# Kernel tuning notes

Measured on AMD Instinct MI355X. Metric: run time of the kernel, lower is better.

The kernel has to match this reference:

```python
import jax, jax.numpy as jnp
import numpy as np

VOCAB = 50000
D = 256          # vector_dim == hidden size
SEQ = 128
BATCH = 4096
NUM_CLASSES = 5


def setup_inputs() -> dict:
    key = jax.random.key(0)
    ks = jax.random.split(key, 8)
    x = jax.random.randint(ks[0], (BATCH, SEQ), 0, VOCAB, dtype=jnp.int64)
    scale = 1.0 / np.sqrt(D)
    emb = jax.random.normal(ks[1], (VOCAB, D), dtype=jnp.float32)
    emb = emb.at[0].set(0.0)  # padding_idx=0 row is zero
    W_ih = jax.random.uniform(ks[2], (D, D), jnp.float32, -scale, scale)
    W_hh = jax.random.uniform(ks[3], (D, D), jnp.float32, -scale, scale)
    b_ih = jax.random.uniform(ks[4], (D,), jnp.float32, -scale, scale)
    b_hh = jax.random.uniform(ks[5], (D,), jnp.float32, -scale, scale)
    W_cls = jax.random.uniform(ks[6], (NUM_CLASSES, D), jnp.float32, -scale, scale)
    b_cls = jax.random.uniform(ks[7], (NUM_CLASSES,), jnp.float32, -scale, scale)
    return {"x": x, "emb": emb, "W_ih": W_ih, "W_hh": W_hh,
            "b_ih": b_ih, "b_hh": b_hh, "W_cls": W_cls, "b_cls": b_cls}


def reference(x, emb, W_ih, W_hh, b_ih, b_hh, W_cls, b_cls):
    # Embedding lookup: [B, S, D]
    xe = emb[x]
    # Precompute input projections for all timesteps in one GEMM.
    x_proj = jnp.einsum("bsd,hd->bsh", xe, W_ih) + b_ih + b_hh  # [B, S, D]

    def step(h, xp_t):
        h = jnp.tanh(xp_t + h @ W_hh.T)
        return h, None

    h0 = jnp.zeros((x.shape[0], W_hh.shape[0]), dtype=xe.dtype)
    # scan over time axis: [S, B, D]
    h_last, _ = jax.lax.scan(step, h0, jnp.swapaxes(x_proj, 0, 1))
    # classifier on last step
    return h_last @ W_cls.T + b_cls  # [B, 5]
```

## Files before the change

### kernel.cpp

```cpp
#include <hip/hip_runtime.h>


typedef __attribute__((ext_vector_type(8))) short bf16x8;
typedef __attribute__((ext_vector_type(4))) float f32x4;

#define VOCAB 50000
#define NBLK_EMB 256
#define LDS_STRIDE 264

__device__ __align__(256) unsigned short g_P[VOCAB * 256];

static __device__ __forceinline__ float bf2f(unsigned short u) {
    union { unsigned int i; float f; } v; v.i = ((unsigned int)u) << 16; return v.f;
}
static __device__ __forceinline__ float bfbits2f(unsigned int zext_u16) {
    union { unsigned int i; float f; } v; v.i = zext_u16 << 16; return v.f;
}
static __device__ __forceinline__ unsigned short f2bf_rne(float f) {
    union { float f; unsigned int i; } v; v.f = f;
    unsigned int r = v.i + 0x7FFFu + ((v.i >> 16) & 1u);
    return (unsigned short)(r >> 16);
}
static __device__ __forceinline__ unsigned short f2bf_fast(float f) {
    union { float f; unsigned int i; } v; v.f = f;
    return (unsigned short)((v.i + 0x8000u) >> 16);
}
static __device__ __forceinline__ bf16x8 cvt8(float4 a, float4 b) {
    bf16x8 r;
    r[0] = (short)f2bf_rne(a.x); r[1] = (short)f2bf_rne(a.y);
    r[2] = (short)f2bf_rne(a.z); r[3] = (short)f2bf_rne(a.w);
    r[4] = (short)f2bf_rne(b.x); r[5] = (short)f2bf_rne(b.y);
    r[6] = (short)f2bf_rne(b.z); r[7] = (short)f2bf_rne(b.w);
    return r;
}
static __device__ __forceinline__ bf16x8 load8_bf(const float* __restrict__ p) {
    return cvt8(((const float4*)p)[0], ((const float4*)p)[1]);
}
static __device__ __forceinline__ float fast_tanh(float x) {
    x = __builtin_amdgcn_fmed3f(x, -8.f, 8.f);
    float e = __expf(2.f * x);
    return __builtin_fmaf(-2.f, __builtin_amdgcn_rcpf(e + 1.f), 1.f);
}

__global__ __launch_bounds__(256)
void emb_proj_kernel(const float* __restrict__ emb,
                     const float* __restrict__ W_ih,
                     const float* __restrict__ b_ih,
                     const float* __restrict__ b_hh)
{
    __shared__ __align__(16) unsigned short tin [16 * LDS_STRIDE];
    __shared__ __align__(16) unsigned short tout[16 * LDS_STRIDE];
    const int tid  = threadIdx.x;
    const int lane = tid & 63;
    const int wid  = tid >> 6;
    const int n0   = wid * 64;
    const int row  = tid >> 4, seg = tid & 15;

    bf16x8 wf[4][8];
    float  bias[4];
    #pragma unroll
    for (int nt = 0; nt < 4; ++nt) {
        int n = n0 + nt * 16 + (lane & 15);
        bias[nt] = b_ih[n] + b_hh[n];
        #pragma unroll
        for (int kt = 0; kt < 8; ++kt)
            wf[nt][kt] = load8_bf(W_ih + n * 256 + (lane >> 4) * 8 + kt * 32);
    }

    int tile = blockIdx.x;
    float4 a0, a1, a2, a3;
    {
        const float4* s = (const float4*)(emb + ((size_t)tile * 16 + row) * 256 + seg * 16);
        a0 = s[0]; a1 = s[1]; a2 = s[2]; a3 = s[3];
    }

    for (; tile < 3125; tile += NBLK_EMB) {
        *(bf16x8*)(&tin[row * LDS_STRIDE + seg * 16])     = cvt8(a0, a1);
        *(bf16x8*)(&tin[row * LDS_STRIDE + seg * 16 + 8]) = cvt8(a2, a3);
        int tn = tile + NBLK_EMB;
        if (tn < 3125) {
            const float4* s = (const float4*)(emb + ((size_t)tn * 16 + row) * 256 + seg * 16);
            a0 = s[0]; a1 = s[1]; a2 = s[2]; a3 = s[3];
        }
        __syncthreads();

        f32x4 acc[4];
        #pragma unroll
        for (int nt = 0; nt < 4; ++nt) acc[nt] = (f32x4){0.f, 0.f, 0.f, 0.f};
        #pragma unroll
        for (int kt = 0; kt < 8; ++kt) {
            bf16x8 a = *(bf16x8*)(&tin[(lane & 15) * LDS_STRIDE + (lane >> 4) * 8 + kt * 32]);
            #pragma unroll
            for (int nt = 0; nt < 4; ++nt)
                acc[nt] = __builtin_amdgcn_mfma_f32_16x16x32_bf16(a, wf[nt][kt], acc[nt], 0, 0, 0);
        }
        #pragma unroll
        for (int nt = 0; nt < 4; ++nt) {
            int n = n0 + nt * 16 + (lane & 15);
            #pragma unroll
            for (int r = 0; r < 4; ++r)
                tout[((lane >> 4) * 4 + r) * LDS_STRIDE + n] = f2bf_rne(acc[nt][r] + bias[nt]);
        }
        __syncthreads();
        {
            uint4 o0 = *(uint4*)(&tout[row * LDS_STRIDE + seg * 16]);
            uint4 o1 = *(uint4*)(&tout[row * LDS_STRIDE + seg * 16 + 8]);
            uint4* dst = (uint4*)(g_P + ((size_t)tile * 16 + row) * 256 + seg * 16);
            dst[0] = o0; dst[1] = o1;
        }
    }
}

__global__ __launch_bounds__(512, 2)
void rnn_kernel(const int* __restrict__ x,
                const float* __restrict__ W_hh,
                const float* __restrict__ W_cls,
                const float* __restrict__ b_cls,
                float* __restrict__ out)
{
    __shared__ __align__(16) unsigned short h_lds[2][16 * 256];
    __shared__ __align__(16) int tok_t[128 * 16];
    __shared__ __align__(16) float wcls_lds[5 * 256];
    __shared__ float bcls_lds[5];

    const int tid  = threadIdx.x;
    const int lane = tid & 63;
    const int wid  = tid >> 6;
    const int b0   = blockIdx.x * 16;
    const int n0   = wid * 32;
    const int l15  = lane & 15;
    const int quad = lane >> 4;

    bf16x8 wf[2][8];
    #pragma unroll
    for (int nt = 0; nt < 2; ++nt) {
        int n = n0 + nt * 16 + l15;
        #pragma unroll
        for (int kt = 0; kt < 8; ++kt)
            wf[nt][kt] = load8_bf(W_hh + n * 256 + quad * 8 + kt * 32);
    }

    {
        int row = tid & 15, tq = tid >> 4;
        int4 v = *(const int4*)(x + (size_t)(b0 + row) * 128 + tq * 4);
        tok_t[(tq * 4 + 0) * 16 + row] = v.x;
        tok_t[(tq * 4 + 1) * 16 + row] = v.y;
        tok_t[(tq * 4 + 2) * 16 + row] = v.z;
        tok_t[(tq * 4 + 3) * 16 + row] = v.w;
    }
    if (tid < 320) ((float4*)wcls_lds)[tid] = ((const float4*)W_cls)[tid];
    if (tid < 5)   bcls_lds[tid] = b_cls[tid];
    #pragma unroll
    for (int i = 0; i < 4; ++i) ((unsigned int*)h_lds[0])[tid + i * 512] = 0;

    int aoff[8];
    #pragma unroll
    for (int kt = 0; kt < 8; ++kt)
        aoff[kt] = l15 * 512 + (((quad + 4 * kt) ^ l15) << 4);
    int woff[8];
    #pragma unroll
    for (int nt = 0; nt < 2; ++nt)
        #pragma unroll
        for (int r = 0; r < 4; ++r) {
            int row = quad * 4 + r;
            int g   = (n0 >> 3) + nt * 2 + (l15 >> 3);
            woff[nt * 4 + r] = row * 512 + ((g ^ row) << 4) + (l15 & 7) * 2;
        }

    const unsigned int colByte = (unsigned int)(n0 + l15) * 2;

    unsigned int gA[8], gB[8];
    #pragma unroll
    for (int r = 0; r < 4; ++r) {
        const int* xr = x + (size_t)(b0 + quad * 4 + r) * 128;
        const unsigned short* p0 = g_P + (size_t)xr[0] * 256 + n0 + l15;
        const unsigned short* p1 = g_P + (size_t)xr[1] * 256 + n0 + l15;
        gA[r] = p0[0]; gA[4 + r] = p0[16];
        gB[r] = p1[0]; gB[4 + r] = p1[16];
    }
    __syncthreads();

    char* const h0 = (char*)&h_lds[0][0];

    auto step = [&](const char* hA, char* hW, unsigned int* g, int t) {
        f32x4 acc0 = { bfbits2f(g[0]), bfbits2f(g[1]), bfbits2f(g[2]), bfbits2f(g[3]) };
        f32x4 acc1 = { bfbits2f(g[4]), bfbits2f(g[5]), bfbits2f(g[6]), bfbits2f(g[7]) };
        if (t + 2 < 128) {
            int4 tk = *(const int4*)&tok_t[(t + 2) * 16 + quad * 4];
            const unsigned short* r0 = (const unsigned short*)((const char*)g_P + ((unsigned int)tk.x * 512 + colByte));
            const unsigned short* r1 = (const unsigned short*)((const char*)g_P + ((unsigned int)tk.y * 512 + colByte));
            const unsigned short* r2 = (const unsigned short*)((const char*)g_P + ((unsigned int)tk.z * 512 + colByte));
            const unsigned short* r3 = (const unsigned short*)((const char*)g_P + ((unsigned int)tk.w * 512 + colByte));
            g[0] = r0[0]; g[4] = r0[16];
            g[1] = r1[0]; g[5] = r1[16];
            g[2] = r2[0]; g[6] = r2[16];
            g[3] = r3[0]; g[7] = r3[16];
        }
        #pragma unroll
        for (int kt = 0; kt < 8; ++kt) {
            bf16x8 a = *(const bf16x8*)(hA + aoff[kt]);
            acc0 = __builtin_amdgcn_mfma_f32_16x16x32_bf16(a, wf[0][kt], acc0, 0, 0, 0);
            acc1 = __builtin_amdgcn_mfma_f32_16x16x32_bf16(a, wf[1][kt], acc1, 0, 0, 0);
        }
        #pragma unroll
        for (int r = 0; r < 4; ++r) {
            *(unsigned short*)(hW + woff[r])     = f2bf_fast(fast_tanh(acc0[r]));
            *(unsigned short*)(hW + woff[4 + r]) = f2bf_fast(fast_tanh(acc1[r]));
        }
    };

    #pragma unroll 1
    for (int t2 = 0; t2 < 64; ++t2) {
        step(h0,        h0 + 8192, gA, 2 * t2);
        __syncthreads();
        step(h0 + 8192, h0,        gB, 2 * t2 + 1);
        __syncthreads();
    }

    if (tid < 320) {
        int q = tid & 3, p = tid >> 2;
        int row = p / 5, c = p - row * 5;
        float acc = 0.f;
        #pragma unroll
        for (int kk = 0; kk < 64; ++kk) {
            int k = q * 64 + kk;
            int off = row * 512 + ((((k >> 3) ^ row)) << 4) + (k & 7) * 2;
            acc += bf2f(*(const unsigned short*)(h0 + off)) * wcls_lds[c * 256 + k];
        }
        acc += __shfl_xor(acc, 1);
        acc += __shfl_xor(acc, 2);
        if (q == 0) out[(size_t)(b0 + row) * 5 + c] = acc + bcls_lds[c];
    }
}

extern "C" void kernel_launch(void* const* d_in, const int* in_sizes, int n_in,
                              void* d_out, int out_size, void* d_ws, size_t ws_size,
                              hipStream_t stream)
{
    const int*   x     = (const int*)d_in[0];
    const float* emb   = (const float*)d_in[1];
    const float* W_ih  = (const float*)d_in[2];
    const float* W_hh  = (const float*)d_in[3];
    const float* b_ih  = (const float*)d_in[4];
    const float* b_hh  = (const float*)d_in[5];
    const float* W_cls = (const float*)d_in[6];
    const float* b_cls = (const float*)d_in[7];
    float*       out   = (float*)d_out;
    (void)d_ws; (void)ws_size;

    emb_proj_kernel<<<NBLK_EMB, 256, 0, stream>>>(emb, W_ih, b_ih, b_hh);
    rnn_kernel<<<256, 512, 0, stream>>>(x, W_hh, W_cls, b_cls, out);
}
```

Before: 226.1 us.

## Stage projected-input gathers into LDS via async global_load_lds DMA

Replaces the per-thread scattered 2-byte register gathers of the precomputed input projection with 16-byte global_load_lds transfers into a double-buffered LDS tile. Each step issues the next timestep's row fetch, then waits on vmcnt before the barrier, and reads the current timestep's values from LDS through a skewed layout. This cuts the number of tiny global loads per step, but prefetch depth shrinks from two steps to one, and a full vmcnt wait now sits on the serial recurrence path.

```diff
diff --git a/kernel.cpp b/kernel.cpp
--- a/kernel.cpp
+++ b/kernel.cpp
@@ -12,9 +12,6 @@
 
 static __device__ __forceinline__ float bf2f(unsigned short u) {
     union { unsigned int i; float f; } v; v.i = ((unsigned int)u) << 16; return v.f;
-}
-static __device__ __forceinline__ float bfbits2f(unsigned int zext_u16) {
-    union { unsigned int i; float f; } v; v.i = zext_u16 << 16; return v.f;
 }
 static __device__ __forceinline__ unsigned short f2bf_rne(float f) {
     union { float f; unsigned int i; } v; v.f = f;
@@ -40,6 +37,14 @@
     x = __builtin_amdgcn_fmed3f(x, -8.f, 8.f);
     float e = __expf(2.f * x);
     return __builtin_fmaf(-2.f, __builtin_amdgcn_rcpf(e + 1.f), 1.f);
+}
+static __device__ __forceinline__ void dma16(const void* g, void* l) {
+    __builtin_amdgcn_global_load_lds(
+        (const __attribute__((address_space(1))) unsigned int*)g,
+        (__attribute__((address_space(3))) unsigned int*)l, 16, 0, 0);
+}
+static __device__ __forceinline__ void wait_vm0() {
+    __builtin_amdgcn_s_waitcnt(0x0f70);
 }
 
 __global__ __launch_bounds__(256)
@@ -118,7 +123,8 @@
                 const float* __restrict__ b_cls,
                 float* __restrict__ out)
 {
-    __shared__ __align__(16) unsigned short h_lds[2][16 * 256];
+    __shared__ __align__(16) unsigned short h_lds [2][16 * 256];
+    __shared__ __align__(16) unsigned short xp_lds[2][16 * 256];
     __shared__ __align__(16) int tok_t[128 * 16];
     __shared__ __align__(16) float wcls_lds[5 * 256];
     __shared__ float bcls_lds[5];
@@ -166,35 +172,41 @@
             int g   = (n0 >> 3) + nt * 2 + (l15 >> 3);
             woff[nt * 4 + r] = row * 512 + ((g ^ row) << 4) + (l15 & 7) * 2;
         }
-
-    const unsigned int colByte = (unsigned int)(n0 + l15) * 2;
-
-    unsigned int gA[8], gB[8];
-    #pragma unroll
-    for (int r = 0; r < 4; ++r) {
-        const int* xr = x + (size_t)(b0 + quad * 4 + r) * 128;
-        const unsigned short* p0 = g_P + (size_t)xr[0] * 256 + n0 + l15;
-        const unsigned short* p1 = g_P + (size_t)xr[1] * 256 + n0 + l15;
-        gA[r] = p0[0]; gA[4 + r] = p0[16];
-        gB[r] = p1[0]; gB[4 + r] = p1[16];
-    }
+    int xoff[8];
+    #pragma unroll
+    for (int nt = 0; nt < 2; ++nt)
+        #pragma unroll
+        for (int r = 0; r < 4; ++r) {
+            int row = quad * 4 + r, c = n0 + nt * 16 + l15;
+            xoff[nt * 4 + r] = (row >> 1) * 1024 + (row & 1) * 512
+                             + ((((c >> 3) + (row >> 1)) & 31) << 4) + (c & 7) * 2;
+        }
+
+    const int dmarow = 2 * wid + (lane >> 5);
+    const unsigned int dmaseg = (unsigned int)(((lane & 31) - wid) & 31);
+    char* const xbase = (char*)&xp_lds[0][0];
+    const int   wofs  = wid << 10;
+
     __syncthreads();
+    {
+        int tok = tok_t[0 * 16 + dmarow];
+        dma16(g_P + (size_t)tok * 256 + dmaseg * 8, xbase + wofs);
+    }
+    wait_vm0();
+    __syncthreads();
 
     char* const h0 = (char*)&h_lds[0][0];
 
-    auto step = [&](const char* hA, char* hW, unsigned int* g, int t) {
-        f32x4 acc0 = { bfbits2f(g[0]), bfbits2f(g[1]), bfbits2f(g[2]), bfbits2f(g[3]) };
-        f32x4 acc1 = { bfbits2f(g[4]), bfbits2f(g[5]), bfbits2f(g[6]), bfbits2f(g[7]) };
-        if (t + 2 < 128) {
-            int4 tk = *(const int4*)&tok_t[(t + 2) * 16 + quad * 4];
-            const unsigned short* r0 = (const unsigned short*)((const char*)g_P + ((unsigned int)tk.x * 512 + colByte));
-            const unsigned short* r1 = (const unsigned short*)((const char*)g_P + ((unsigned int)tk.y * 512 + colByte));
-            const unsigned short* r2 = (const unsigned short*)((const char*)g_P + ((unsigned int)tk.z * 512 + colByte));
-            const unsigned short* r3 = (const unsigned short*)((const char*)g_P + ((unsigned int)tk.w * 512 + colByte));
-            g[0] = r0[0]; g[4] = r0[16];
-            g[1] = r1[0]; g[5] = r1[16];
-            g[2] = r2[0]; g[6] = r2[16];
-            g[3] = r3[0]; g[7] = r3[16];
+    auto step = [&](const char* hA, char* hW, const char* xR, char* gw, int t) {
+        if (t + 1 < 128) {
+            int tok = tok_t[(t + 1) * 16 + dmarow];
+            dma16(g_P + (size_t)tok * 256 + dmaseg * 8, gw + wofs);
+        }
+        f32x4 acc0, acc1;
+        #pragma unroll
+        for (int r = 0; r < 4; ++r) {
+            acc0[r] = bf2f(*(const unsigned short*)(xR + xoff[r]));
+            acc1[r] = bf2f(*(const unsigned short*)(xR + xoff[4 + r]));
         }
         #pragma unroll
         for (int kt = 0; kt < 8; ++kt) {
@@ -211,9 +223,11 @@
 
     #pragma unroll 1
     for (int t2 = 0; t2 < 64; ++t2) {
-        step(h0,        h0 + 8192, gA, 2 * t2);
-        __syncthreads();
-        step(h0 + 8192, h0,        gB, 2 * t2 + 1);
+        step(h0,        h0 + 8192, xbase,        xbase + 8192, 2 * t2);
+        wait_vm0();
+        __syncthreads();
+        step(h0 + 8192, h0,        xbase + 8192, xbase,        2 * t2 + 1);
+        wait_vm0();
         __syncthreads();
     }
 
```

Result: slower. 248.5 us (+9.9%).

## Halve batch rows per RNN block and launch one projection block per tile

Applied to the files above, without the earlier changes.

The RNN kernel now processes 8 batch rows per block instead of 16, doubling the grid to 512 blocks and raising the launch-bounds occupancy hint to 4 blocks per CU. The MFMA still computes 16 rows, with the upper half zero and ignored, and only lanes for the real rows gather projections and write h. The embedding-projection kernel drops its persistent, software-prefetched loop and launches one block per 16-row vocabulary tile. The aim is to spread the sequential recurrence across more CUs and waves, at the cost of wasting half of each MFMA and losing the prefetch overlap in the projection kernel.

```diff
diff --git a/kernel.cpp b/kernel.cpp
--- a/kernel.cpp
+++ b/kernel.cpp
@@ -5,16 +5,12 @@
 typedef __attribute__((ext_vector_type(4))) float f32x4;
 
 #define VOCAB 50000
-#define NBLK_EMB 256
 #define LDS_STRIDE 264
 
 __device__ __align__(256) unsigned short g_P[VOCAB * 256];
 
 static __device__ __forceinline__ float bf2f(unsigned short u) {
     union { unsigned int i; float f; } v; v.i = ((unsigned int)u) << 16; return v.f;
-}
-static __device__ __forceinline__ float bfbits2f(unsigned int zext_u16) {
-    union { unsigned int i; float f; } v; v.i = zext_u16 << 16; return v.f;
 }
 static __device__ __forceinline__ unsigned short f2bf_rne(float f) {
     union { float f; unsigned int i; } v; v.f = f;
@@ -55,6 +51,7 @@
     const int wid  = tid >> 6;
     const int n0   = wid * 64;
     const int row  = tid >> 4, seg = tid & 15;
+    const int v0   = blockIdx.x * 16;
 
     bf16x8 wf[4][8];
     float  bias[4];
@@ -67,51 +64,41 @@
             wf[nt][kt] = load8_bf(W_ih + n * 256 + (lane >> 4) * 8 + kt * 32);
     }
 
-    int tile = blockIdx.x;
-    float4 a0, a1, a2, a3;
     {
-        const float4* s = (const float4*)(emb + ((size_t)tile * 16 + row) * 256 + seg * 16);
-        a0 = s[0]; a1 = s[1]; a2 = s[2]; a3 = s[3];
-    }
-
-    for (; tile < 3125; tile += NBLK_EMB) {
-        *(bf16x8*)(&tin[row * LDS_STRIDE + seg * 16])     = cvt8(a0, a1);
-        *(bf16x8*)(&tin[row * LDS_STRIDE + seg * 16 + 8]) = cvt8(a2, a3);
-        int tn = tile + NBLK_EMB;
-        if (tn < 3125) {
-            const float4* s = (const float4*)(emb + ((size_t)tn * 16 + row) * 256 + seg * 16);
-            a0 = s[0]; a1 = s[1]; a2 = s[2]; a3 = s[3];
-        }
-        __syncthreads();
-
-        f32x4 acc[4];
-        #pragma unroll
-        for (int nt = 0; nt < 4; ++nt) acc[nt] = (f32x4){0.f, 0.f, 0.f, 0.f};
-        #pragma unroll
-        for (int kt = 0; kt < 8; ++kt) {
-            bf16x8 a = *(bf16x8*)(&tin[(lane & 15) * LDS_STRIDE + (lane >> 4) * 8 + kt * 32]);
-            #pragma unroll
-            for (int nt = 0; nt < 4; ++nt)
-                acc[nt] = __builtin_amdgcn_mfma_f32_16x16x32_bf16(a, wf[nt][kt], acc[nt], 0, 0, 0);
-        }
-        #pragma unroll
-        for (int nt = 0; nt < 4; ++nt) {
-            int n = n0 + nt * 16 + (lane & 15);
-            #pragma unroll
-            for (int r = 0; r < 4; ++r)
-                tout[((lane >> 4) * 4 + r) * LDS_STRIDE + n] = f2bf_rne(acc[nt][r] + bias[nt]);
-        }
-        __syncthreads();
-        {
-            uint4 o0 = *(uint4*)(&tout[row * LDS_STRIDE + seg * 16]);
-            uint4 o1 = *(uint4*)(&tout[row * LDS_STRIDE + seg * 16 + 8]);
-            uint4* dst = (uint4*)(g_P + ((size_t)tile * 16 + row) * 256 + seg * 16);
-            dst[0] = o0; dst[1] = o1;
-        }
-    }
-}
-
-__global__ __launch_bounds__(512, 2)
+        const float* src = emb + (size_t)(v0 + row) * 256 + seg * 16;
+        bf16x8 lo = load8_bf(src), hi = load8_bf(src + 8);
+        *(bf16x8*)(&tin[row * LDS_STRIDE + seg * 16])     = lo;
+        *(bf16x8*)(&tin[row * LDS_STRIDE + seg * 16 + 8]) = hi;
+    }
+    __syncthreads();
+
+    f32x4 acc[4];
+    #pragma unroll
+    for (int nt = 0; nt < 4; ++nt) acc[nt] = (f32x4){0.f, 0.f, 0.f, 0.f};
+    #pragma unroll
+    for (int kt = 0; kt < 8; ++kt) {
+        bf16x8 a = *(bf16x8*)(&tin[(lane & 15) * LDS_STRIDE + (lane >> 4) * 8 + kt * 32]);
+        #pragma unroll
+        for (int nt = 0; nt < 4; ++nt)
+            acc[nt] = __builtin_amdgcn_mfma_f32_16x16x32_bf16(a, wf[nt][kt], acc[nt], 0, 0, 0);
+    }
+    #pragma unroll
+    for (int nt = 0; nt < 4; ++nt) {
+        int n = n0 + nt * 16 + (lane & 15);
+        #pragma unroll
+        for (int r = 0; r < 4; ++r)
+            tout[((lane >> 4) * 4 + r) * LDS_STRIDE + n] = f2bf_rne(acc[nt][r] + bias[nt]);
+    }
+    __syncthreads();
+    {
+        uint4 o0 = *(uint4*)(&tout[row * LDS_STRIDE + seg * 16]);
+        uint4 o1 = *(uint4*)(&tout[row * LDS_STRIDE + seg * 16 + 8]);
+        uint4* dst = (uint4*)(g_P + (size_t)(v0 + row) * 256 + seg * 16);
+        dst[0] = o0; dst[1] = o1;
+    }
+}
+
+__global__ __launch_bounds__(512, 4)
 void rnn_kernel(const int* __restrict__ x,
                 const float* __restrict__ W_hh,
                 const float* __restrict__ W_cls,
@@ -119,14 +106,14 @@
                 float* __restrict__ out)
 {
     __shared__ __align__(16) unsigned short h_lds[2][16 * 256];
-    __shared__ __align__(16) int tok_t[128 * 16];
+    __shared__ __align__(16) int tok_t[128 * 8];
     __shared__ __align__(16) float wcls_lds[5 * 256];
     __shared__ float bcls_lds[5];
 
     const int tid  = threadIdx.x;
     const int lane = tid & 63;
     const int wid  = tid >> 6;
-    const int b0   = blockIdx.x * 16;
+    const int b0   = blockIdx.x * 8;
     const int n0   = wid * 32;
     const int l15  = lane & 15;
     const int quad = lane >> 4;
@@ -140,18 +127,18 @@
             wf[nt][kt] = load8_bf(W_hh + n * 256 + quad * 8 + kt * 32);
     }
 
-    {
-        int row = tid & 15, tq = tid >> 4;
+    if (tid < 256) {
+        int row = tid & 7, tq = tid >> 3;
         int4 v = *(const int4*)(x + (size_t)(b0 + row) * 128 + tq * 4);
-        tok_t[(tq * 4 + 0) * 16 + row] = v.x;
-        tok_t[(tq * 4 + 1) * 16 + row] = v.y;
-        tok_t[(tq * 4 + 2) * 16 + row] = v.z;
-        tok_t[(tq * 4 + 3) * 16 + row] = v.w;
+        tok_t[(tq * 4 + 0) * 8 + row] = v.x;
+        tok_t[(tq * 4 + 1) * 8 + row] = v.y;
+        tok_t[(tq * 4 + 2) * 8 + row] = v.z;
+        tok_t[(tq * 4 + 3) * 8 + row] = v.w;
     }
     if (tid < 320) ((float4*)wcls_lds)[tid] = ((const float4*)W_cls)[tid];
     if (tid < 5)   bcls_lds[tid] = b_cls[tid];
     #pragma unroll
-    for (int i = 0; i < 4; ++i) ((unsigned int*)h_lds[0])[tid + i * 512] = 0;
+    for (int i = 0; i < 8; ++i) ((unsigned int*)h_lds[0])[tid + i * 512] = 0;
 
     int aoff[8];
     #pragma unroll
@@ -167,26 +154,32 @@
             woff[nt * 4 + r] = row * 512 + ((g ^ row) << 4) + (l15 & 7) * 2;
         }
 
+    unsigned int gA[8] = {0,0,0,0,0,0,0,0};
+    unsigned int gB[8] = {0,0,0,0,0,0,0,0};
+    if (quad < 2) {
+        #pragma unroll
+        for (int r = 0; r < 4; ++r) {
+            const int* xr = x + (size_t)(b0 + quad * 4 + r) * 128;
+            const unsigned short* p0 = g_P + (size_t)xr[0] * 256 + n0 + l15;
+            const unsigned short* p1 = g_P + (size_t)xr[1] * 256 + n0 + l15;
+            gA[r] = p0[0]; gA[4 + r] = p0[16];
+            gB[r] = p1[0]; gB[4 + r] = p1[16];
+        }
+    }
+    __syncthreads();
+
+    char* const h0 = (char*)&h_lds[0][0];
     const unsigned int colByte = (unsigned int)(n0 + l15) * 2;
 
-    unsigned int gA[8], gB[8];
-    #pragma unroll
-    for (int r = 0; r < 4; ++r) {
-        const int* xr = x + (size_t)(b0 + quad * 4 + r) * 128;
-        const unsigned short* p0 = g_P + (size_t)xr[0] * 256 + n0 + l15;
-        const unsigned short* p1 = g_P + (size_t)xr[1] * 256 + n0 + l15;
-        gA[r] = p0[0]; gA[4 + r] = p0[16];
-        gB[r] = p1[0]; gB[4 + r] = p1[16];
-    }
-    __syncthreads();
-
-    char* const h0 = (char*)&h_lds[0][0];
-
     auto step = [&](const char* hA, char* hW, unsigned int* g, int t) {
-        f32x4 acc0 = { bfbits2f(g[0]), bfbits2f(g[1]), bfbits2f(g[2]), bfbits2f(g[3]) };
-        f32x4 acc1 = { bfbits2f(g[4]), bfbits2f(g[5]), bfbits2f(g[6]), bfbits2f(g[7]) };
-        if (t + 2 < 128) {
-            int4 tk = *(const int4*)&tok_t[(t + 2) * 16 + quad * 4];
+        f32x4 acc0, acc1;
+        #pragma unroll
+        for (int r = 0; r < 4; ++r) {
+            acc0[r] = bf2f((unsigned short)g[r]);
+            acc1[r] = bf2f((unsigned short)g[4 + r]);
+        }
+        if (quad < 2 && t + 2 < 128) {
+            int4 tk = *(const int4*)&tok_t[(t + 2) * 8 + quad * 4];
             const unsigned short* r0 = (const unsigned short*)((const char*)g_P + ((unsigned int)tk.x * 512 + colByte));
             const unsigned short* r1 = (const unsigned short*)((const char*)g_P + ((unsigned int)tk.y * 512 + colByte));
             const unsigned short* r2 = (const unsigned short*)((const char*)g_P + ((unsigned int)tk.z * 512 + colByte));
@@ -202,10 +195,12 @@
             acc0 = __builtin_amdgcn_mfma_f32_16x16x32_bf16(a, wf[0][kt], acc0, 0, 0, 0);
             acc1 = __builtin_amdgcn_mfma_f32_16x16x32_bf16(a, wf[1][kt], acc1, 0, 0, 0);
         }
-        #pragma unroll
-        for (int r = 0; r < 4; ++r) {
-            *(unsigned short*)(hW + woff[r])     = f2bf_fast(fast_tanh(acc0[r]));
-            *(unsigned short*)(hW + woff[4 + r]) = f2bf_fast(fast_tanh(acc1[r]));
+        if (quad < 2) {
+            #pragma unroll
+            for (int r = 0; r < 4; ++r) {
+                *(unsigned short*)(hW + woff[r])     = f2bf_fast(fast_tanh(acc0[r]));
+                *(unsigned short*)(hW + woff[4 + r]) = f2bf_fast(fast_tanh(acc1[r]));
+            }
         }
     };
 
@@ -217,7 +212,7 @@
         __syncthreads();
     }
 
-    if (tid < 320) {
+    if (tid < 160) {
         int q = tid & 3, p = tid >> 2;
         int row = p / 5, c = p - row * 5;
         float acc = 0.f;
@@ -248,6 +243,6 @@
     float*       out   = (float*)d_out;
     (void)d_ws; (void)ws_size;
 
-    emb_proj_kernel<<<NBLK_EMB, 256, 0, stream>>>(emb, W_ih, b_ih, b_hh);
-    rnn_kernel<<<256, 512, 0, stream>>>(x, W_hh, W_cls, b_cls, out);
-}
+    emb_proj_kernel<<<3125, 256, 0, stream>>>(emb, W_ih, b_ih, b_hh);
+    rnn_kernel<<<512, 512, 0, stream>>>(x, W_hh, W_cls, b_cls, out);
+}
```

Measured after the change: 378.6 us. 67.4% more time.

## Deepen gather prefetch in RNN loop and widen embedding projection grid

Applied to the files above, without the earlier changes.

The recurrent kernel now prefetches the precomputed projection rows for four timesteps at a time into double-buffered register chunks, so gathers are issued further ahead and have more latency to hide behind the per-step MFMA work. The embedding projection kernel moves to 512 threads per block with 8 waves each covering 32 output columns, and to a larger grid of 1024 blocks for more parallelism in the precompute. The deeper prefetch raises register pressure in the RNN kernel, which runs under a 512x2 launch bound and could spill.

```diff
diff --git a/kernel.cpp b/kernel.cpp
--- a/kernel.cpp
+++ b/kernel.cpp
@@ -5,16 +5,13 @@
 typedef __attribute__((ext_vector_type(4))) float f32x4;
 
 #define VOCAB 50000
-#define NBLK_EMB 256
+#define NBLK_EMB 1024
 #define LDS_STRIDE 264
 
 __device__ __align__(256) unsigned short g_P[VOCAB * 256];
 
 static __device__ __forceinline__ float bf2f(unsigned short u) {
     union { unsigned int i; float f; } v; v.i = ((unsigned int)u) << 16; return v.f;
-}
-static __device__ __forceinline__ float bfbits2f(unsigned int zext_u16) {
-    union { unsigned int i; float f; } v; v.i = zext_u16 << 16; return v.f;
 }
 static __device__ __forceinline__ unsigned short f2bf_rne(float f) {
     union { float f; unsigned int i; } v; v.f = f;
@@ -42,7 +39,7 @@
     return __builtin_fmaf(-2.f, __builtin_amdgcn_rcpf(e + 1.f), 1.f);
 }
 
-__global__ __launch_bounds__(256)
+__global__ __launch_bounds__(512)
 void emb_proj_kernel(const float* __restrict__ emb,
                      const float* __restrict__ W_ih,
                      const float* __restrict__ b_ih,
@@ -53,60 +50,58 @@
     const int tid  = threadIdx.x;
     const int lane = tid & 63;
     const int wid  = tid >> 6;
-    const int n0   = wid * 64;
-    const int row  = tid >> 4, seg = tid & 15;
-
-    bf16x8 wf[4][8];
-    float  bias[4];
-    #pragma unroll
-    for (int nt = 0; nt < 4; ++nt) {
-        int n = n0 + nt * 16 + (lane & 15);
+    const int n0   = wid * 32;
+    const int l15  = lane & 15;
+    const int quad = lane >> 4;
+    const int row  = tid >> 5, seg = tid & 31;
+
+    bf16x8 wf[2][8];
+    float  bias[2];
+    #pragma unroll
+    for (int nt = 0; nt < 2; ++nt) {
+        int n = n0 + nt * 16 + l15;
         bias[nt] = b_ih[n] + b_hh[n];
         #pragma unroll
         for (int kt = 0; kt < 8; ++kt)
-            wf[nt][kt] = load8_bf(W_ih + n * 256 + (lane >> 4) * 8 + kt * 32);
+            wf[nt][kt] = load8_bf(W_ih + n * 256 + quad * 8 + kt * 32);
     }
 
     int tile = blockIdx.x;
-    float4 a0, a1, a2, a3;
+    float4 a0, a1;
     {
-        const float4* s = (const float4*)(emb + ((size_t)tile * 16 + row) * 256 + seg * 16);
-        a0 = s[0]; a1 = s[1]; a2 = s[2]; a3 = s[3];
+        const float4* s = (const float4*)(emb + ((size_t)tile * 16 + row) * 256 + seg * 8);
+        a0 = s[0]; a1 = s[1];
     }
 
     for (; tile < 3125; tile += NBLK_EMB) {
-        *(bf16x8*)(&tin[row * LDS_STRIDE + seg * 16])     = cvt8(a0, a1);
-        *(bf16x8*)(&tin[row * LDS_STRIDE + seg * 16 + 8]) = cvt8(a2, a3);
+        *(bf16x8*)(&tin[row * LDS_STRIDE + seg * 8]) = cvt8(a0, a1);
         int tn = tile + NBLK_EMB;
         if (tn < 3125) {
-            const float4* s = (const float4*)(emb + ((size_t)tn * 16 + row) * 256 + seg * 16);
-            a0 = s[0]; a1 = s[1]; a2 = s[2]; a3 = s[3];
+            const float4* s = (const float4*)(emb + ((size_t)tn * 16 + row) * 256 + seg * 8);
+            a0 = s[0]; a1 = s[1];
         }
         __syncthreads();
 
-        f32x4 acc[4];
-        #pragma unroll
-        for (int nt = 0; nt < 4; ++nt) acc[nt] = (f32x4){0.f, 0.f, 0.f, 0.f};
+        f32x4 acc[2];
+        acc[0] = (f32x4){0.f, 0.f, 0.f, 0.f};
+        acc[1] = (f32x4){0.f, 0.f, 0.f, 0.f};
         #pragma unroll
         for (int kt = 0; kt < 8; ++kt) {
-            bf16x8 a = *(bf16x8*)(&tin[(lane & 15) * LDS_STRIDE + (lane >> 4) * 8 + kt * 32]);
-            #pragma unroll
-            for (int nt = 0; nt < 4; ++nt)
-                acc[nt] = __builtin_amdgcn_mfma_f32_16x16x32_bf16(a, wf[nt][kt], acc[nt], 0, 0, 0);
-        }
-        #pragma unroll
-        for (int nt = 0; nt < 4; ++nt) {
-            int n = n0 + nt * 16 + (lane & 15);
+            bf16x8 a = *(bf16x8*)(&tin[l15 * LDS_STRIDE + quad * 8 + kt * 32]);
+            acc[0] = __builtin_amdgcn_mfma_f32_16x16x32_bf16(a, wf[0][kt], acc[0], 0, 0, 0);
+            acc[1] = __builtin_amdgcn_mfma_f32_16x16x32_bf16(a, wf[1][kt], acc[1], 0, 0, 0);
+        }
+        #pragma unroll
+        for (int nt = 0; nt < 2; ++nt) {
+            int n = n0 + nt * 16 + l15;
             #pragma unroll
             for (int r = 0; r < 4; ++r)
-                tout[((lane >> 4) * 4 + r) * LDS_STRIDE + n] = f2bf_rne(acc[nt][r] + bias[nt]);
+                tout[(quad * 4 + r) * LDS_STRIDE + n] = f2bf_rne(acc[nt][r] + bias[nt]);
         }
         __syncthreads();
         {
-            uint4 o0 = *(uint4*)(&tout[row * LDS_STRIDE + seg * 16]);
-            uint4 o1 = *(uint4*)(&tout[row * LDS_STRIDE + seg * 16 + 8]);
-            uint4* dst = (uint4*)(g_P + ((size_t)tile * 16 + row) * 256 + seg * 16);
-            dst[0] = o0; dst[1] = o1;
+            uint4 o = *(uint4*)(&tout[row * LDS_STRIDE + seg * 8]);
+            *(uint4*)(g_P + ((size_t)tile * 16 + row) * 256 + seg * 8) = o;
         }
     }
 }
@@ -169,32 +164,41 @@
 
     const unsigned int colByte = (unsigned int)(n0 + l15) * 2;
 
-    unsigned int gA[8], gB[8];
-    #pragma unroll
-    for (int r = 0; r < 4; ++r) {
-        const int* xr = x + (size_t)(b0 + quad * 4 + r) * 128;
-        const unsigned short* p0 = g_P + (size_t)xr[0] * 256 + n0 + l15;
-        const unsigned short* p1 = g_P + (size_t)xr[1] * 256 + n0 + l15;
-        gA[r] = p0[0]; gA[4 + r] = p0[16];
-        gB[r] = p1[0]; gB[4 + r] = p1[16];
-    }
+    unsigned int gb[2][4][8];
+
+    #pragma unroll
+    for (int p = 0; p < 4; ++p)
+        #pragma unroll
+        for (int j = 0; j < 4; ++j) {
+            int tok = x[(size_t)(b0 + quad * 4 + j) * 128 + p];
+            const unsigned short* pp = g_P + (size_t)tok * 256 + n0 + l15;
+            gb[0][p][j] = pp[0]; gb[0][p][4 + j] = pp[16];
+        }
     __syncthreads();
 
     char* const h0 = (char*)&h_lds[0][0];
 
-    auto step = [&](const char* hA, char* hW, unsigned int* g, int t) {
-        f32x4 acc0 = { bfbits2f(g[0]), bfbits2f(g[1]), bfbits2f(g[2]), bfbits2f(g[3]) };
-        f32x4 acc1 = { bfbits2f(g[4]), bfbits2f(g[5]), bfbits2f(g[6]), bfbits2f(g[7]) };
-        if (t + 2 < 128) {
-            int4 tk = *(const int4*)&tok_t[(t + 2) * 16 + quad * 4];
+    auto issue_chunk = [&](int b, int tbase) {
+        #pragma unroll
+        for (int p = 0; p < 4; ++p) {
+            int4 tk = *(const int4*)&tok_t[(tbase + p) * 16 + quad * 4];
             const unsigned short* r0 = (const unsigned short*)((const char*)g_P + ((unsigned int)tk.x * 512 + colByte));
             const unsigned short* r1 = (const unsigned short*)((const char*)g_P + ((unsigned int)tk.y * 512 + colByte));
             const unsigned short* r2 = (const unsigned short*)((const char*)g_P + ((unsigned int)tk.z * 512 + colByte));
             const unsigned short* r3 = (const unsigned short*)((const char*)g_P + ((unsigned int)tk.w * 512 + colByte));
-            g[0] = r0[0]; g[4] = r0[16];
-            g[1] = r1[0]; g[5] = r1[16];
-            g[2] = r2[0]; g[6] = r2[16];
-            g[3] = r3[0]; g[7] = r3[16];
+            gb[b][p][0] = r0[0]; gb[b][p][4] = r0[16];
+            gb[b][p][1] = r1[0]; gb[b][p][5] = r1[16];
+            gb[b][p][2] = r2[0]; gb[b][p][6] = r2[16];
+            gb[b][p][3] = r3[0]; gb[b][p][7] = r3[16];
+        }
+    };
+
+    auto stepf = [&](const char* hA, char* hW, int b, int p) {
+        f32x4 acc0, acc1;
+        #pragma unroll
+        for (int r = 0; r < 4; ++r) {
+            acc0[r] = bf2f((unsigned short)gb[b][p][r]);
+            acc1[r] = bf2f((unsigned short)gb[b][p][4 + r]);
         }
         #pragma unroll
         for (int kt = 0; kt < 8; ++kt) {
@@ -210,11 +214,18 @@
     };
 
     #pragma unroll 1
-    for (int t2 = 0; t2 < 64; ++t2) {
-        step(h0,        h0 + 8192, gA, 2 * t2);
-        __syncthreads();
-        step(h0 + 8192, h0,        gB, 2 * t2 + 1);
-        __syncthreads();
+    for (int i8 = 0; i8 < 16; ++i8) {
+        const int tb = i8 * 8;
+        issue_chunk(1, tb + 4);
+        stepf(h0,        h0 + 8192, 0, 0); __syncthreads();
+        stepf(h0 + 8192, h0,        0, 1); __syncthreads();
+        stepf(h0,        h0 + 8192, 0, 2); __syncthreads();
+        stepf(h0 + 8192, h0,        0, 3); __syncthreads();
+        if (i8 < 15) issue_chunk(0, tb + 8);
+        stepf(h0,        h0 + 8192, 1, 0); __syncthreads();
+        stepf(h0 + 8192, h0,        1, 1); __syncthreads();
+        stepf(h0,        h0 + 8192, 1, 2); __syncthreads();
+        stepf(h0 + 8192, h0,        1, 3); __syncthreads();
     }
 
     if (tid < 320) {
@@ -248,6 +259,6 @@
     float*       out   = (float*)d_out;
     (void)d_ws; (void)ws_size;
 
-    emb_proj_kernel<<<NBLK_EMB, 256, 0, stream>>>(emb, W_ih, b_ih, b_hh);
+    emb_proj_kernel<<<NBLK_EMB, 512, 0, stream>>>(emb, W_ih, b_ih, b_hh);
     rnn_kernel<<<256, 512, 0, stream>>>(x, W_hh, W_cls, b_cls, out);
 }
```

Result: slower. 238.7 us (+5.6%).
